# Kernel optimization log

Measured on AMD Instinct MI355X. Metric: run time of the kernel, lower is better.

The kernel has to match this reference:

```python
import jax, jax.numpy as jnp
import numpy as np

B_, L, D_MODEL = 2, 2048, 1024
EXPAND, D_INNER, D_STATE, DT_RANK, D_CONV = 2, 2048, 16, 64, 4
DT_MIN, DT_MAX = 0.001, 0.1


def setup_inputs() -> dict:
    key = jax.random.key(0)
    ks = jax.random.split(key, 8)
    s = lambda fan: 1.0 / np.sqrt(fan)
    # S4D-real style init for A: A = -exp(A_log), A_log = log(1..n) repeated over d_inner
    A0 = jnp.broadcast_to(jnp.arange(1, D_STATE + 1, dtype=jnp.float32), (D_INNER, D_STATE))
    return {
        "x": jax.random.normal(ks[0], (B_, L, D_MODEL), jnp.float32),
        "W_in": jax.random.normal(ks[1], (D_MODEL, 2 * D_INNER), jnp.float32) * s(D_MODEL),
        "conv_k": jax.random.normal(ks[2], (D_CONV, D_INNER // EXPAND, D_INNER), jnp.float32) * s(D_CONV * D_INNER // EXPAND),
        "conv_b": jnp.zeros((D_INNER,), jnp.float32),
        "W_x": jax.random.normal(ks[3], (D_INNER, DT_RANK + 2 * D_STATE), jnp.float32) * s(D_INNER),
        "W_dt": jax.random.normal(ks[4], (DT_RANK, D_INNER), jnp.float32) * s(DT_RANK),
        "b_dt": jnp.zeros((D_INNER,), jnp.float32),
        "A_log": jnp.log(A0),
        "D": jnp.ones((D_INNER,), jnp.float32),
        "W_out": jax.random.normal(ks[5], (D_INNER, D_MODEL), jnp.float32) * s(D_INNER),
    }


def reference(x, W_in, conv_k, conv_b, W_x, W_dt, b_dt, A_log, D, W_out):
    # in_proj -> split into ssm branch and gating residual branch
    xz = x @ W_in                                   # (b, l, 2*d_inner)
    xs, res = jnp.split(xz, 2, axis=-1)
    # causal grouped conv1d (feature_group_count = expand)
    xc = jax.lax.conv_general_dilated(
        xs, conv_k, window_strides=(1,), padding=[(D_CONV - 1, 0)],
        dimension_numbers=("NWC", "WIO", "NWC"), feature_group_count=EXPAND,
    ) + conv_b
    u = jax.nn.silu(xc)                             # (b, l, d_inner)
    # x_proj -> delta(low-rank), B, C
    dbc = u @ W_x                                   # (b, l, dt_rank + 2n)
    dt_raw = dbc[..., :DT_RANK]
    Bm = dbc[..., DT_RANK:DT_RANK + D_STATE]        # (b, l, n)
    Cm = dbc[..., DT_RANK + D_STATE:]               # (b, l, n)
    delta = jax.nn.softplus(dt_raw @ W_dt + b_dt)   # (b, l, d_inner)
    delta = jnp.clip(delta, DT_MIN, DT_MAX)
    A = -jnp.exp(A_log)                             # (d_inner, n)
    dA = jnp.exp(delta[..., None] * A)              # (b, l, d_inner, n)
    dBu = delta[..., None] * u[..., None] * Bm[:, :, None, :]  # (b, l, d_inner, n)

    def step(h, inp):
        dA_t, dBu_t, C_t = inp                      # (b,d,n),(b,d,n),(b,n)
        h = dA_t * h + dBu_t
        y_t = jnp.einsum('bdn,bn->bd', h, C_t)
        return h, y_t

    h0 = jnp.zeros((x.shape[0], D_INNER, D_STATE), dA.dtype)
    _, y = jax.lax.scan(step, h0, (dA.transpose(1, 0, 2, 3), dBu.transpose(1, 0, 2, 3), Cm.transpose(1, 0, 2)))
    y = y.transpose(1, 0, 2) + u * D                # (b, l, d_inner)
    out = (y * jax.nn.silu(res)) @ W_out            # (b, l, d_model)
    return out
```

## Files before the change

### kernel.cpp

```cpp
#include <hip/hip_runtime.h>
#include <math.h>


typedef unsigned short ushort_t;
typedef unsigned int uint_t;
typedef __bf16 bf16x8 __attribute__((ext_vector_type(8)));
typedef float floatx4 __attribute__((ext_vector_type(4)));

#define LDS_STRIDE 40

#define GLOAD16(gp, lp) \
    __builtin_amdgcn_global_load_lds((const __attribute__((address_space(1))) void*)(gp), \
                                     (__attribute__((address_space(3))) void*)(lp), 16, 0, 0)

__device__ __forceinline__ float silu_f(float x) { return x / (1.0f + __expf(-x)); }

__device__ __forceinline__ unsigned short f2bf(float f) {
    unsigned u = __float_as_uint(f);
    unsigned r = u + 0x7fffu + ((u >> 16) & 1u);
    return (unsigned short)(r >> 16);
}
__device__ __forceinline__ float bf2f(unsigned short h) {
    return __uint_as_float(((unsigned)h) << 16);
}
__device__ __forceinline__ uint_t packhl(float v) {
    const unsigned short h = f2bf(v);
    const unsigned short l = f2bf(v - bf2f(h));
    return (uint_t)h | ((uint_t)l << 16);
}
__device__ __forceinline__ float unpack_sum(uint_t pk) {
    return __uint_as_float(pk << 16) + __uint_as_float(pk & 0xffff0000u);
}
__device__ __forceinline__ void unpack8(uint4 w0, uint4 w1, uint4& H, uint4& L) {
    H.x = (w0.x & 0xffffu) | (w0.y << 16);  L.x = (w0.x >> 16) | (w0.y & 0xffff0000u);
    H.y = (w0.z & 0xffffu) | (w0.w << 16);  L.y = (w0.z >> 16) | (w0.w & 0xffff0000u);
    H.z = (w1.x & 0xffffu) | (w1.y << 16);  L.z = (w1.x >> 16) | (w1.y & 0xffff0000u);
    H.w = (w1.z & 0xffffu) | (w1.w << 16);  L.w = (w1.z >> 16) | (w1.w & 0xffff0000u);
}
__device__ __forceinline__ size_t faddr(int n, int k, int KC) {
    return ((size_t)((n >> 4) * KC + (k >> 5)) * 64 + (n & 15) + (((k >> 3) & 3) << 4)) * 8
           + (k & 7);
}

__global__ __launch_bounds__(256) void prep_all(
    const float* __restrict__ x, const float* __restrict__ W_in,
    const float* __restrict__ conv_k, const float* __restrict__ W_out,
    const float* __restrict__ W_x,
    uint_t* __restrict__ xpk,
    ushort_t* __restrict__ WinF, ushort_t* __restrict__ convkF,
    ushort_t* __restrict__ WoutF, ushort_t* __restrict__ WxF,
    ushort_t* __restrict__ XSP_h)
{
    __shared__ float ts[32][33];
    const int bid = blockIdx.x;
    const int t = threadIdx.x;
    if (bid < 4096) {
        const size_t i4 = ((size_t)bid * 256 + t) * 4;
        float4 v = *(const float4*)&x[i4];
        uint4 pk;
        pk.x = packhl(v.x); pk.y = packhl(v.y); pk.z = packhl(v.z); pk.w = packhl(v.w);
        *(uint4*)&xpk[i4] = pk;
        return;
    }
    if (bid >= 18432 && bid < 19456) {
        const int idx = (bid - 18432) * 256 + t;
        const int r = idx >> 11, k = idx & 2047;
        float v = (r < 96) ? W_x[(size_t)k * 96 + r] : 0.f;
        WxF[faddr(r, k, 64)] = f2bf(v);
        return;
    }
    if (bid >= 19456) {
        const int idx = (bid - 19456) * 256 + t;
        const int b = idx / 6144, rem = idx % 6144;
        const int lp = rem >> 11, c = rem & 2047;
        XSP_h[((size_t)b * 2051 + lp) * 2048 + c] = 0;
        return;
    }
    const float* src; int R, C, KC; ushort_t* dst; int bx, by;
    if (bid < 8192)       { src = W_in;   R = 1024; C = 4096; KC = 32;  dst = WinF;
                            int l = bid - 4096;  bx = l & 127; by = l >> 7; }
    else if (bid < 16384) { src = conv_k; R = 4096; C = 2048; KC = 128; dst = convkF;
                            int l = bid - 8192;  bx = l & 63;  by = l >> 6; }
    else                  { src = W_out;  R = 2048; C = 1024; KC = 64;  dst = WoutF;
                            int l = bid - 16384; bx = l & 31;  by = l >> 5; }
    const int tx = t & 31, ty = t >> 5;
    const int r0 = by * 32, c0 = bx * 32;
    #pragma unroll
    for (int j = 0; j < 4; ++j)
        ts[ty + j * 8][tx] = src[(size_t)(r0 + ty + j * 8) * C + c0 + tx];
    __syncthreads();
    #pragma unroll
    for (int j = 0; j < 4; ++j) {
        const int n = c0 + ty + j * 8, k = r0 + tx;
        dst[faddr(n, k, KC)] = f2bf(ts[tx][ty + j * 8]);
    }
}

template<int MODE>
__global__ __launch_bounds__(256) void gemm2(
    const uint_t* __restrict__ Apk, const ushort_t* __restrict__ Bf, int Kfull,
    float* __restrict__ Cf, ushort_t* __restrict__ Oh)
{
    __shared__ __align__(16) ushort_t As_h[128 * LDS_STRIDE];
    __shared__ __align__(16) ushort_t As_l[128 * LDS_STRIDE];
    const int t = threadIdx.x;
    int bx, by;
    if (MODE == 2) { bx = blockIdx.x; by = blockIdx.y; }
    else {
        const int lin = blockIdx.x, xcd = lin & 7, s = lin >> 3;
        bx = s >> 2;
        by = xcd * 4 + (s & 3);
    }
    const int m0 = by * 128;
    const int n0 = (MODE == 2) ? 0 : bx * 128;
    const int kbeg = (MODE == 2) ? bx * 512 : 0;
    const int kend = (MODE == 2) ? kbeg + 512 : Kfull;
    const int KC = Kfull >> 5;
    const int lane = t & 63, wave = t >> 6;
    const int wm = (wave >> 1) * 64, wn = (wave & 1) * 64;
    const int m16 = lane & 15, q = lane >> 4;
    const int n16b = (n0 + wn) >> 4;
    const int r_0 = t >> 2, cc_0 = (t & 3) * 8;
    const int r_1 = (t + 256) >> 2, cc_1 = ((t + 256) & 3) * 8;

    uint4 a00 = *(const uint4*)&Apk[(size_t)(m0 + r_0) * Kfull + kbeg + cc_0];
    uint4 a01 = *(const uint4*)&Apk[(size_t)(m0 + r_0) * Kfull + kbeg + cc_0 + 4];
    uint4 a10 = *(const uint4*)&Apk[(size_t)(m0 + r_1) * Kfull + kbeg + cc_1];
    uint4 a11 = *(const uint4*)&Apk[(size_t)(m0 + r_1) * Kfull + kbeg + cc_1 + 4];
    bf16x8 bc[4];
    {
        const int kc = kbeg >> 5;
        #pragma unroll
        for (int j = 0; j < 4; ++j)
            bc[j] = *(const bf16x8*)&Bf[(((size_t)(n16b + j) * KC + kc) * 64 + lane) * 8];
    }

    floatx4 acc[4][4];
    const floatx4 zz = {0.f, 0.f, 0.f, 0.f};
    #pragma unroll
    for (int i = 0; i < 4; ++i)
        #pragma unroll
        for (int j = 0; j < 4; ++j) acc[i][j] = zz;

    for (int k0 = kbeg; k0 < kend; k0 += 32) {
        uint4 H, L;
        unpack8(a00, a01, H, L);
        *(uint4*)&As_h[r_0 * LDS_STRIDE + cc_0] = H;
        *(uint4*)&As_l[r_0 * LDS_STRIDE + cc_0] = L;
        unpack8(a10, a11, H, L);
        *(uint4*)&As_h[r_1 * LDS_STRIDE + cc_1] = H;
        *(uint4*)&As_l[r_1 * LDS_STRIDE + cc_1] = L;
        __syncthreads();
        bf16x8 bn[4];
        if (k0 + 32 < kend) {
            const int kn = k0 + 32, kc = kn >> 5;
            a00 = *(const uint4*)&Apk[(size_t)(m0 + r_0) * Kfull + kn + cc_0];
            a01 = *(const uint4*)&Apk[(size_t)(m0 + r_0) * Kfull + kn + cc_0 + 4];
            a10 = *(const uint4*)&Apk[(size_t)(m0 + r_1) * Kfull + kn + cc_1];
            a11 = *(const uint4*)&Apk[(size_t)(m0 + r_1) * Kfull + kn + cc_1 + 4];
            #pragma unroll
            for (int j = 0; j < 4; ++j)
                bn[j] = *(const bf16x8*)&Bf[(((size_t)(n16b + j) * KC + kc) * 64 + lane) * 8];
        }
        bf16x8 ah[4], al[4];
        #pragma unroll
        for (int i = 0; i < 4; ++i) {
            const int off = (wm + i * 16 + m16) * LDS_STRIDE + q * 8;
            ah[i] = *(const bf16x8*)&As_h[off];
            al[i] = *(const bf16x8*)&As_l[off];
        }
        #pragma unroll
        for (int i = 0; i < 4; ++i)
            #pragma unroll
            for (int j = 0; j < 4; ++j) {
                acc[i][j] = __builtin_amdgcn_mfma_f32_16x16x32_bf16(ah[i], bc[j], acc[i][j], 0, 0, 0);
                acc[i][j] = __builtin_amdgcn_mfma_f32_16x16x32_bf16(al[i], bc[j], acc[i][j], 0, 0, 0);
            }
        #pragma unroll
        for (int j = 0; j < 4; ++j) bc[j] = bn[j];
        __syncthreads();
    }

    float* Cp = (MODE == 2) ? (Cf + (size_t)bx * 393216) : Cf;
    #pragma unroll
    for (int i = 0; i < 4; ++i) {
        const int row_b = m0 + wm + i * 16 + q * 4;
        #pragma unroll
        for (int j = 0; j < 4; ++j) {
            const int col = n0 + wn + j * 16 + m16;
            #pragma unroll
            for (int rr = 0; rr < 4; ++rr) {
                const int row = row_b + rr;
                const float v = acc[i][j][rr];
                if (MODE == 0) {
                    if (n0 < 2048) {
                        const int b = row >> 11, l = row & 2047;
                        Oh[((size_t)b * 2051 + l + 3) * 2048 + col] = f2bf(v);
                    } else {
                        Cp[(size_t)row * 2048 + (col - 2048)] = v;
                    }
                } else if (MODE == 1) {
                    Cp[(size_t)row * 1024 + col] = v;
                } else {
                    if (col < 96) Cp[(size_t)row * 96 + col] = v;
                }
            }
        }
    }
}

__global__ __launch_bounds__(512, 4) void conv2(
    const ushort_t* __restrict__ Xh, const ushort_t* __restrict__ Bf,
    const float* __restrict__ bias, uint_t* __restrict__ Upk)
{
    __shared__ __align__(16) ushort_t Asw[2][2][128 * 32];
    __shared__ __align__(16) ushort_t Bsw[2][2][8 * 512];
    const int t = threadIdx.x;
    const int lin = blockIdx.x, xcd = lin & 7, s = lin >> 3;
    const int sweep = s >> 5, r = s & 31;
    const int bxp = r >> 1;
    const int by = xcd * 4 + ((sweep << 1) | (r & 1));
    const int m0 = by * 128, n0 = bxp * 128;
    const int g1024 = (n0 >= 1024) ? 1024 : 0;
    const int lane = t & 63, wave = t >> 6;
    const int wm = (wave >> 2) * 64, wn = (wave & 3) * 32;
    const int m16 = lane & 15, q = lane >> 4;
    const int n16base = n0 >> 4;
    const int Xrow0 = (m0 >> 11) * 2051 + (m0 & 2047);
    const int l16 = lane >> 2;
    const int csA = (lane & 3) ^ ((lane >> 3) & 3);

    auto stageT = [&](int dbuf, int kcL, int Tn) {
        const int wtap = Tn >> 4;
        const int i0 = ((Tn << 6) & 1023) + kcL * 32;
        const int kc = Tn * 2 + kcL;
        {
            const int r0 = wave * 16;
            const size_t gidx = (size_t)(Xrow0 + r0 + l16 + wtap) * 2048
                              + g1024 + i0 + csA * 8;
            GLOAD16(Xh + gidx, &Asw[dbuf][kcL][r0 * 32]);
        }
        {
            const size_t gidx = ((size_t)(n16base + wave) * 128 + kc) * 512 + lane * 8;
            GLOAD16(Bf + gidx, &Bsw[dbuf][kcL][wave * 512]);
        }
    };

    floatx4 acc[4][2];
    const floatx4 zz = {0.f, 0.f, 0.f, 0.f};
    #pragma unroll
    for (int i = 0; i < 4; ++i)
        #pragma unroll
        for (int j = 0; j < 2; ++j) acc[i][j] = zz;

    bf16x8 a0[4], b0[2], a1[4], b1[2];

    auto readA = [&](int dbuf, int kcL, bf16x8 (&ah)[4]) {
        #pragma unroll
        for (int mi = 0; mi < 4; ++mi) {
            const int rr2 = wm + mi * 16 + m16;
            const int ch = q ^ ((m16 >> 1) & 3);
            ah[mi] = *(const bf16x8*)&Asw[dbuf][kcL][rr2 * 32 + ch * 8];
        }
    };
    auto readB = [&](int dbuf, int kcL, bf16x8 (&bb)[2]) {
        #pragma unroll
        for (int j = 0; j < 2; ++j)
            bb[j] = *(const bf16x8*)&Bsw[dbuf][kcL][((wn >> 4) + j) * 512 + lane * 8];
    };
    auto mfma8 = [&](bf16x8 (&ah)[4], bf16x8 (&bb)[2]) {
        __builtin_amdgcn_s_setprio(1);
        #pragma unroll
        for (int mi = 0; mi < 4; ++mi)
            #pragma unroll
            for (int j = 0; j < 2; ++j)
                acc[mi][j] = __builtin_amdgcn_mfma_f32_16x16x32_bf16(ah[mi], bb[j], acc[mi][j], 0, 0, 0);
        __builtin_amdgcn_s_setprio(0);
    };

    stageT(0, 0, 0);
    stageT(0, 1, 0);
    asm volatile("s_waitcnt vmcnt(2)" ::: "memory");
    __builtin_amdgcn_s_barrier();
    asm volatile("" ::: "memory");
    readA(0, 0, a0); readB(0, 0, b0);

    int cur = 0;
    for (int T = 0; T < 64; ++T) {
        const int nxt = cur ^ 1;
        if (T < 63) {
            stageT(nxt, 0, T + 1);
            asm volatile("s_waitcnt vmcnt(2)" ::: "memory");
        } else {
            asm volatile("s_waitcnt vmcnt(0)" ::: "memory");
        }
        __builtin_amdgcn_s_barrier();
        asm volatile("" ::: "memory");
        readA(cur, 1, a1); readB(cur, 1, b1);
        mfma8(a0, b0);
        if (T < 63) stageT(nxt, 1, T + 1);
        mfma8(a1, b1);
        asm volatile("" ::: "memory");
        if (T < 63) {
            asm volatile("s_waitcnt vmcnt(2)" ::: "memory");
            __builtin_amdgcn_s_barrier();
            asm volatile("" ::: "memory");
            readA(nxt, 0, a0); readB(nxt, 0, b0);
        }
        cur = nxt;
    }

    #pragma unroll
    for (int i = 0; i < 4; ++i) {
        const int row_b = m0 + wm + i * 16 + q * 4;
        #pragma unroll
        for (int j = 0; j < 2; ++j) {
            const int col = n0 + wn + j * 16 + m16;
            const float bz = bias[col];
            #pragma unroll
            for (int rr = 0; rr < 4; ++rr) {
                const int row = row_b + rr;
                const float v = silu_f(acc[i][j][rr] + bz);
                Upk[(size_t)row * 2048 + col] = packhl(v);
            }
        }
    }
}

__global__ __launch_bounds__(256) void dbc_reduce(
    const float* __restrict__ DBCP, float* __restrict__ DBC)
{
    const int i = blockIdx.x * 256 + threadIdx.x;
    DBC[i] = (DBCP[i] + DBCP[393216 + i]) + (DBCP[786432 + i] + DBCP[1179648 + i]);
}

__global__ __launch_bounds__(256) void delta_kernel(
    const float* __restrict__ DBC, const float* __restrict__ W_dt,
    const float* __restrict__ b_dt, float* __restrict__ DELTA)
{
    const int n  = blockIdx.x * 256 + threadIdx.x;
    const int p0 = blockIdx.y * 16;
    const int t  = threadIdx.x;
    __shared__ float dt_s[16][64];
    #pragma unroll
    for (int j = 0; j < 4; ++j) {
        const int lin = j * 256 + t;
        const int r = lin >> 6, k = lin & 63;
        dt_s[r][k] = DBC[(size_t)(p0 + r) * 96 + k];
    }
    __syncthreads();
    float acc[16];
    const float bz = b_dt[n];
    #pragma unroll
    for (int r = 0; r < 16; ++r) acc[r] = bz;
    for (int k = 0; k < 64; ++k) {
        const float wv = W_dt[(size_t)k * 2048 + n];
        #pragma unroll
        for (int r = 0; r < 16; ++r) acc[r] += dt_s[r][k] * wv;
    }
    #pragma unroll
    for (int r = 0; r < 16; ++r) {
        float a = acc[r];
        float sp = (a > 20.f) ? a : log1pf(expf(a));
        sp = fminf(fmaxf(sp, 0.001f), 0.1f);
        DELTA[(size_t)(p0 + r) * 2048 + n] = sp;
    }
}

__global__ __launch_bounds__(256) void scan_p1(
    const float* __restrict__ DELTA, const uint_t* __restrict__ Upk,
    const float* __restrict__ DBC, const float* __restrict__ A_log,
    float* __restrict__ HEND, float* __restrict__ SD)
{
    const int t = threadIdx.x;
    const int d = blockIdx.x * 256 + t;
    const int c = blockIdx.y;
    const int b = blockIdx.z;
    const int p0 = b * 2048 + c * 32;
    __shared__ float Bs[32][16];
    for (int lin = t; lin < 512; lin += 256) {
        const int s = lin >> 4, n = lin & 15;
        Bs[s][n] = DBC[(size_t)(p0 + s) * 96 + 64 + n];
    }
    __syncthreads();
    float Af[16];
    *(float4*)&Af[0]  = *(const float4*)&A_log[(size_t)d * 16 + 0];
    *(float4*)&Af[4]  = *(const float4*)&A_log[(size_t)d * 16 + 4];
    *(float4*)&Af[8]  = *(const float4*)&A_log[(size_t)d * 16 + 8];
    *(float4*)&Af[12] = *(const float4*)&A_log[(size_t)d * 16 + 12];
    #pragma unroll
    for (int n = 0; n < 16; ++n) Af[n] = -__expf(Af[n]);

    float h[16] = {};
    float sd = 0.f;
    for (int s = 0; s < 32; ++s) {
        const size_t ix = (size_t)(p0 + s) * 2048 + d;
        const float dv = DELTA[ix];
        const float uv = unpack_sum(Upk[ix]);
        const float du = dv * uv;
        sd += dv;
        #pragma unroll
        for (int n = 0; n < 16; ++n)
            h[n] = __expf(dv * Af[n]) * h[n] + du * Bs[s][n];
    }
    const size_t hb = (((size_t)c * 2 + b) * 2048 + d) * 16;
    *(float4*)&HEND[hb + 0]  = *(float4*)&h[0];
    *(float4*)&HEND[hb + 4]  = *(float4*)&h[4];
    *(float4*)&HEND[hb + 8]  = *(float4*)&h[8];
    *(float4*)&HEND[hb + 12] = *(float4*)&h[12];
    SD[((size_t)c * 2 + b) * 2048 + d] = sd;
}

__global__ __launch_bounds__(256) void scan_p2(
    const float* __restrict__ HEND, const float* __restrict__ SD,
    const float* __restrict__ A_log, float* __restrict__ HINIT)
{
    const int g = blockIdx.x * 256 + threadIdx.x;
    const int n = g & 15, d = (g >> 4) & 2047, b = (g >> 15) & 1;
    const float Af = -__expf(A_log[(size_t)d * 16 + n]);
    float h = 0.f;
    #pragma unroll 8
    for (int c = 0; c < 64; ++c) {
        const size_t cb = (size_t)c * 2 + b;
        const size_t idx = (cb * 2048 + d) * 16 + n;
        HINIT[idx] = h;
        h = __expf(Af * SD[cb * 2048 + d]) * h + HEND[idx];
    }
}

__global__ __launch_bounds__(256) void scan_p3(
    const float* __restrict__ DELTA, const uint_t* __restrict__ Upk,
    const float* __restrict__ DBC, const float* __restrict__ RES,
    const float* __restrict__ A_log, const float* __restrict__ Dp,
    const float* __restrict__ HINIT, uint_t* __restrict__ Gpk)
{
    const int t = threadIdx.x;
    const int d = blockIdx.x * 256 + t;
    const int c = blockIdx.y;
    const int b = blockIdx.z;
    const int p0 = b * 2048 + c * 32;
    __shared__ float Bs[32][16];
    __shared__ float Cs[32][16];
    for (int lin = t; lin < 512; lin += 256) {
        const int s = lin >> 4, n = lin & 15;
        Bs[s][n] = DBC[(size_t)(p0 + s) * 96 + 64 + n];
        Cs[s][n] = DBC[(size_t)(p0 + s) * 96 + 80 + n];
    }
    __syncthreads();
    float Af[16];
    *(float4*)&Af[0]  = *(const float4*)&A_log[(size_t)d * 16 + 0];
    *(float4*)&Af[4]  = *(const float4*)&A_log[(size_t)d * 16 + 4];
    *(float4*)&Af[8]  = *(const float4*)&A_log[(size_t)d * 16 + 8];
    *(float4*)&Af[12] = *(const float4*)&A_log[(size_t)d * 16 + 12];
    #pragma unroll
    for (int n = 0; n < 16; ++n) Af[n] = -__expf(Af[n]);

    const size_t hb = (((size_t)c * 2 + b) * 2048 + d) * 16;
    float h[16];
    *(float4*)&h[0]  = *(const float4*)&HINIT[hb + 0];
    *(float4*)&h[4]  = *(const float4*)&HINIT[hb + 4];
    *(float4*)&h[8]  = *(const float4*)&HINIT[hb + 8];
    *(float4*)&h[12] = *(const float4*)&HINIT[hb + 12];
    const float Dd = Dp[d];

    for (int s = 0; s < 32; ++s) {
        const int p = p0 + s;
        const size_t ix = (size_t)p * 2048 + d;
        const float dv = DELTA[ix];
        const float uv = unpack_sum(Upk[ix]);
        const float du = dv * uv;
        float y = 0.f;
        #pragma unroll
        for (int n = 0; n < 16; ++n) {
            h[n] = __expf(dv * Af[n]) * h[n] + du * Bs[s][n];
            y += h[n] * Cs[s][n];
        }
        const float resv = RES[ix];
        const float gv = (y + uv * Dd) * silu_f(resv);
        Gpk[ix] = packhl(gv);
    }
}

extern "C" void kernel_launch(void* const* d_in, const int* in_sizes, int n_in,
                              void* d_out, int out_size, void* d_ws, size_t ws_size,
                              hipStream_t stream) {
    const float* x      = (const float*)d_in[0];
    const float* W_in   = (const float*)d_in[1];
    const float* conv_k = (const float*)d_in[2];
    const float* conv_b = (const float*)d_in[3];
    const float* W_x    = (const float*)d_in[4];
    const float* W_dt   = (const float*)d_in[5];
    const float* b_dt   = (const float*)d_in[6];
    const float* A_log  = (const float*)d_in[7];
    const float* Dv     = (const float*)d_in[8];
    const float* W_out  = (const float*)d_in[9];
    float* out = (float*)d_out;

    char* base = (char*)d_ws;
    float*    RES      = (float*)(base);
    uint_t*   Upk      = (uint_t*)(base + 33554432);
    float*    DELTA    = (float*)(base + 67108864);
    ushort_t* XSP_h    = (ushort_t*)(base + 100663296);
    float*    HEND     = (float*)(base + 100663296);
    uint_t*   xpk      = (uint_t*)(base + 117465088);
    ushort_t* convkF   = (ushort_t*)(base + 134242304);
    uint_t*   Gpk      = (uint_t*)(base + 117465088);
    ushort_t* WinF     = (ushort_t*)(base + 151019520);
    ushort_t* WoutF    = (ushort_t*)(base + 159408128);
    ushort_t* WxF      = (ushort_t*)(base + 163602432);
    float*    DBCP     = (float*)(base + 164126720);
    float*    DBC      = (float*)(base + 170418176);
    float*    SD       = (float*)(base + 171991040);
    float*    HINIT    = (float*)(base + 173039616);

    prep_all<<<19504, 256, 0, stream>>>(x, W_in, conv_k, W_out, W_x,
                                        xpk, WinF, convkF, WoutF, WxF, XSP_h);
    gemm2<0><<<1024, 256, 0, stream>>>(xpk, WinF, 1024, RES, XSP_h);
    conv2<<<512, 512, 0, stream>>>(XSP_h, convkF, conv_b, Upk);
    gemm2<2><<<dim3(4, 32), 256, 0, stream>>>(Upk, WxF, 2048, DBCP, nullptr);
    dbc_reduce<<<1536, 256, 0, stream>>>(DBCP, DBC);
    delta_kernel<<<dim3(8, 256), 256, 0, stream>>>(DBC, W_dt, b_dt, DELTA);
    scan_p1<<<dim3(8, 64, 2), 256, 0, stream>>>(DELTA, Upk, DBC, A_log, HEND, SD);
    scan_p2<<<256, 256, 0, stream>>>(HEND, SD, A_log, HINIT);
    scan_p3<<<dim3(8, 64, 2), 256, 0, stream>>>(DELTA, Upk, DBC, RES, A_log, Dv,
                                                HINIT, Gpk);
    gemm2<1><<<256, 256, 0, stream>>>(Gpk, WoutF, 2048, out, nullptr);
}
```

Measured before the change: 489.1 us.

## Load conv2 B fragments directly into registers instead of staging through LDS

In the conv2 GEMM kernel, the weight (B) tiles no longer go to shared memory through global_load_lds. Each wave now loads its own pre-swizzled B fragments straight from global memory into registers one step ahead, using ping-pong register buffers and a loop unrolled by two. This cuts LDS traffic and the B-side LDS reads, and halves LDS use, which may help occupancy. In exchange it adds register pressure and needs hand-tuned vmcnt counts, and if those counts are wrong it could race.

```diff
diff --git a/kernel.cpp b/kernel.cpp
--- a/kernel.cpp
+++ b/kernel.cpp
@@ -12,6 +12,7 @@
 #define GLOAD16(gp, lp) \
     __builtin_amdgcn_global_load_lds((const __attribute__((address_space(1))) void*)(gp), \
                                      (__attribute__((address_space(3))) void*)(lp), 16, 0, 0)
+#define FENCE() asm volatile("" ::: "memory")
 
 __device__ __forceinline__ float silu_f(float x) { return x / (1.0f + __expf(-x)); }
 
@@ -214,7 +215,6 @@
     const float* __restrict__ bias, uint_t* __restrict__ Upk)
 {
     __shared__ __align__(16) ushort_t Asw[2][2][128 * 32];
-    __shared__ __align__(16) ushort_t Bsw[2][2][8 * 512];
     const int t = threadIdx.x;
     const int lin = blockIdx.x, xcd = lin & 7, s = lin >> 3;
     const int sweep = s >> 5, r = s & 31;
@@ -225,24 +225,27 @@
     const int lane = t & 63, wave = t >> 6;
     const int wm = (wave >> 2) * 64, wn = (wave & 3) * 32;
     const int m16 = lane & 15, q = lane >> 4;
-    const int n16base = n0 >> 4;
+    const int n16w = (n0 + wn) >> 4;
     const int Xrow0 = (m0 >> 11) * 2051 + (m0 & 2047);
     const int l16 = lane >> 2;
     const int csA = (lane & 3) ^ ((lane >> 3) & 3);
 
-    auto stageT = [&](int dbuf, int kcL, int Tn) {
+    auto stageA = [&](int dbuf, int kcL, int Tn) {
         const int wtap = Tn >> 4;
         const int i0 = ((Tn << 6) & 1023) + kcL * 32;
-        const int kc = Tn * 2 + kcL;
-        {
-            const int r0 = wave * 16;
-            const size_t gidx = (size_t)(Xrow0 + r0 + l16 + wtap) * 2048
-                              + g1024 + i0 + csA * 8;
-            GLOAD16(Xh + gidx, &Asw[dbuf][kcL][r0 * 32]);
-        }
-        {
-            const size_t gidx = ((size_t)(n16base + wave) * 128 + kc) * 512 + lane * 8;
-            GLOAD16(Bf + gidx, &Bsw[dbuf][kcL][wave * 512]);
+        const int r0 = wave * 16;
+        const size_t gidx = (size_t)(Xrow0 + r0 + l16 + wtap) * 2048
+                          + g1024 + i0 + csA * 8;
+        GLOAD16(Xh + gidx, &Asw[dbuf][kcL][r0 * 32]);
+    };
+    auto loadB = [&](int Tn, bf16x8 (&bb)[4]) {
+        #pragma unroll
+        for (int h = 0; h < 2; ++h) {
+            const int kc = Tn * 2 + h;
+            #pragma unroll
+            for (int j = 0; j < 2; ++j)
+                bb[h * 2 + j] =
+                    *(const bf16x8*)&Bf[(((size_t)(n16w + j) * 128 + kc) * 64 + lane) * 8];
         }
     };
 
@@ -253,7 +256,7 @@
         #pragma unroll
         for (int j = 0; j < 2; ++j) acc[i][j] = zz;
 
-    bf16x8 a0[4], b0[2], a1[4], b1[2];
+    bf16x8 a0[4], a1[4], bA[4], bB[4];
 
     auto readA = [&](int dbuf, int kcL, bf16x8 (&ah)[4]) {
         #pragma unroll
@@ -263,51 +266,55 @@
             ah[mi] = *(const bf16x8*)&Asw[dbuf][kcL][rr2 * 32 + ch * 8];
         }
     };
-    auto readB = [&](int dbuf, int kcL, bf16x8 (&bb)[2]) {
-        #pragma unroll
-        for (int j = 0; j < 2; ++j)
-            bb[j] = *(const bf16x8*)&Bsw[dbuf][kcL][((wn >> 4) + j) * 512 + lane * 8];
-    };
-    auto mfma8 = [&](bf16x8 (&ah)[4], bf16x8 (&bb)[2]) {
+    auto mfma8 = [&](bf16x8 (&ah)[4], bf16x8& q0, bf16x8& q1) {
         __builtin_amdgcn_s_setprio(1);
         #pragma unroll
-        for (int mi = 0; mi < 4; ++mi)
-            #pragma unroll
-            for (int j = 0; j < 2; ++j)
-                acc[mi][j] = __builtin_amdgcn_mfma_f32_16x16x32_bf16(ah[mi], bb[j], acc[mi][j], 0, 0, 0);
+        for (int mi = 0; mi < 4; ++mi) {
+            acc[mi][0] = __builtin_amdgcn_mfma_f32_16x16x32_bf16(ah[mi], q0, acc[mi][0], 0, 0, 0);
+            acc[mi][1] = __builtin_amdgcn_mfma_f32_16x16x32_bf16(ah[mi], q1, acc[mi][1], 0, 0, 0);
+        }
         __builtin_amdgcn_s_setprio(0);
     };
 
-    stageT(0, 0, 0);
-    stageT(0, 1, 0);
-    asm volatile("s_waitcnt vmcnt(2)" ::: "memory");
-    __builtin_amdgcn_s_barrier();
-    asm volatile("" ::: "memory");
-    readA(0, 0, a0); readB(0, 0, b0);
-
-    int cur = 0;
-    for (int T = 0; T < 64; ++T) {
-        const int nxt = cur ^ 1;
+    auto body = [&](int T, bf16x8 (&bu)[4], bf16x8 (&bl)[4]) {
+        const int cur = T & 1, nxt = cur ^ 1;
         if (T < 63) {
-            stageT(nxt, 0, T + 1);
-            asm volatile("s_waitcnt vmcnt(2)" ::: "memory");
+            stageA(nxt, 0, T + 1);
+            FENCE();
+            loadB(T + 1, bl);
+            FENCE();
+            asm volatile("s_waitcnt vmcnt(5)" ::: "memory");
         } else {
             asm volatile("s_waitcnt vmcnt(0)" ::: "memory");
         }
         __builtin_amdgcn_s_barrier();
-        asm volatile("" ::: "memory");
-        readA(cur, 1, a1); readB(cur, 1, b1);
-        mfma8(a0, b0);
-        if (T < 63) stageT(nxt, 1, T + 1);
-        mfma8(a1, b1);
-        asm volatile("" ::: "memory");
+        FENCE();
+        readA(cur, 1, a1);
+        mfma8(a0, bu[0], bu[1]);
+        if (T < 63) stageA(nxt, 1, T + 1);
+        mfma8(a1, bu[2], bu[3]);
+        FENCE();
         if (T < 63) {
-            asm volatile("s_waitcnt vmcnt(2)" ::: "memory");
+            asm volatile("s_waitcnt vmcnt(5)" ::: "memory");
             __builtin_amdgcn_s_barrier();
-            asm volatile("" ::: "memory");
-            readA(nxt, 0, a0); readB(nxt, 0, b0);
-        }
-        cur = nxt;
+            FENCE();
+            readA(nxt, 0, a0);
+        }
+    };
+
+    stageA(0, 0, 0);
+    FENCE();
+    loadB(0, bA);
+    FENCE();
+    stageA(0, 1, 0);
+    asm volatile("s_waitcnt vmcnt(5)" ::: "memory");
+    __builtin_amdgcn_s_barrier();
+    FENCE();
+    readA(0, 0, a0);
+
+    for (int T = 0; T < 64; T += 2) {
+        body(T, bA, bB);
+        body(T + 1, bB, bA);
     }
 
     #pragma unroll
```

Measured after the change: 501.9 us. 1.03x slower.
